# Kernel optimization log

Hardware: AMD Instinct MI355X
Metric: run time of the kernel (lower is better)

## Reference

```python
import jax, jax.numpy as jnp
import numpy as np

B, T, IN, H = 4096, 100, 140, 256


def setup_inputs() -> dict:
    key = jax.random.key(0)
    ks = jax.random.split(key, 13)
    s = 1.0 / np.sqrt(H)  # PyTorch LSTM/Linear default init scale
    u = lambda k, shape: jax.random.uniform(k, shape, jnp.float32, -s, s)
    return {
        "x": jax.random.normal(ks[0], (B, T, IN), jnp.float32),
        # LSTM layer 0 (input 140 -> hidden 256), PyTorch gate order i,f,g,o
        "W_ih0": u(ks[1], (4 * H, IN)),
        "W_hh0": u(ks[2], (4 * H, H)),
        "b_ih0": u(ks[3], (4 * H,)),
        "b_hh0": u(ks[4], (4 * H,)),
        # LSTM layer 1 (hidden 256 -> hidden 256)
        "W_ih1": u(ks[5], (4 * H, H)),
        "W_hh1": u(ks[6], (4 * H, H)),
        "b_ih1": u(ks[7], (4 * H,)),
        "b_hh1": u(ks[8], (4 * H,)),
        # advantage MLP: Linear(256,256) -> ReLU -> Linear(256,1)
        "W_a1": u(ks[9], (H, H)),
        "b_a1": u(ks[10], (H,)),
        "W_a2": u(ks[11], (1, H)),
        "b_a2": u(ks[12], (1,)),
    }


def _lstm_cell(xt, h, c, W_ih, W_hh, b):
    # xt: (B, in), h/c: (B, H). PyTorch gate order: i, f, g, o.
    g = xt @ W_ih.T + h @ W_hh.T + b
    i, f, gg, o = jnp.split(g, 4, axis=-1)
    c_new = jax.nn.sigmoid(f) * c + jax.nn.sigmoid(i) * jnp.tanh(gg)
    h_new = jax.nn.sigmoid(o) * jnp.tanh(c_new)
    return h_new, c_new


def reference(x, W_ih0, W_hh0, b_ih0, b_hh0, W_ih1, W_hh1, b_ih1, b_hh1,
              W_a1, b_a1, W_a2, b_a2):
    Bx = x.shape[0]
    b0 = b_ih0 + b_hh0
    b1 = b_ih1 + b_hh1

    def step(carry, xt):
        h0, c0, h1, c1 = carry
        h0, c0 = _lstm_cell(xt, h0, c0, W_ih0, W_hh0, b0)
        h1, c1 = _lstm_cell(h0, h1, c1, W_ih1, W_hh1, b1)
        a = jax.nn.relu(h1 @ W_a1.T + b_a1) @ W_a2.T + b_a2  # (B, 1)
        return (h0, c0, h1, c1), a[:, 0]

    init = tuple(jnp.zeros((Bx, H), x.dtype) for _ in range(4))
    _, outs = jax.lax.scan(step, init, jnp.swapaxes(x, 0, 1))  # (T, B)
    # Faithful to torch.cat(outputs).view(B, -1): flatten in t-major order,
    # then reshape to (B, T) (this scrambles batch/time exactly as the original).
    return outs.reshape(Bx, -1)
```

## Files before the change

kernel.cpp:

```cpp
#include <hip/hip_runtime.h>
#include <cstdint>
#include <cstddef>

#define T_STEPS 100
#define IN_DIM  140
#define HDIM    256
#define BTOT    4096
#define MROWS   16
#define NBLK    (BTOT/MROWS)
#define NTHR    512

typedef _Float16 f16;
typedef _Float16 f16x8 __attribute__((ext_vector_type(8)));
typedef float    f32x4 __attribute__((ext_vector_type(4)));

#define NS0 13
#define NS1 16
#define NSA 8
#define E0 (NS0*64*512)
#define E1 (NS1*64*512)
#define EA (NSA*16*512)
#define F16TOT (E0+E1+EA)
#define EB 2048
#define PREP_TOT (F16TOT+EB)
#define SL (64*512)

#define ACOLS 680
#define H0COL 160
#define H1COL 416

__device__ __forceinline__ float sigmoidf_(float x) {
    return 1.0f / (1.0f + __expf(-x));
}
__device__ __forceinline__ float tanhf_(float x) {
    return 1.0f - 2.0f / (__expf(2.0f * x) + 1.0f);
}

__global__ void prep(const float* __restrict__ Wih0, const float* __restrict__ Whh0,
                     const float* __restrict__ bih0, const float* __restrict__ bhh0,
                     const float* __restrict__ Wih1, const float* __restrict__ Whh1,
                     const float* __restrict__ bih1, const float* __restrict__ bhh1,
                     const float* __restrict__ Wa1,  f16* __restrict__ wsf,
                     float* __restrict__ wsb)
{
    int idx = blockIdx.x * 256 + threadIdx.x;
    if (idx < E0) {
        int e = idx & 7, l = (idx >> 3) & 63, fi = idx >> 9;
        int nt = fi & 63, ks = fi >> 6;
        int k = ks * 32 + ((l >> 4) << 3) + e;
        int n = nt * 16 + (l & 15);
        float v = (k < 160) ? (k < IN_DIM ? Wih0[n * IN_DIM + k] : 0.f)
                            : Whh0[n * HDIM + (k - 160)];
        wsf[idx] = (f16)v;
    } else if (idx < E0 + E1) {
        int i2 = idx - E0;
        int e = i2 & 7, l = (i2 >> 3) & 63, fi = i2 >> 9;
        int nt = fi & 63, ks = fi >> 6;
        int k = ks * 32 + ((l >> 4) << 3) + e;
        int n = nt * 16 + (l & 15);
        float v = (k < HDIM) ? Wih1[n * HDIM + k] : Whh1[n * HDIM + (k - HDIM)];
        wsf[idx] = (f16)v;
    } else if (idx < F16TOT) {
        int i3 = idx - (E0 + E1);
        int e = i3 & 7, l = (i3 >> 3) & 63, fi = i3 >> 9;
        int nt = fi & 15, ks = fi >> 4;
        int k = ks * 32 + ((l >> 4) << 3) + e;
        int j = nt * 16 + (l & 15);
        wsf[idx] = (f16)Wa1[j * HDIM + k];
    } else if (idx < PREP_TOT) {
        int i4 = idx - F16TOT;
        if (i4 < 1024) wsb[i4] = bih0[i4] + bhh0[i4];
        else           wsb[i4] = bih1[i4 - 1024] + bhh1[i4 - 1024];
    }
}

#define GLOAD_LDS(gsrc, ldst)                                              \
    __builtin_amdgcn_global_load_lds(                                      \
        (const __attribute__((address_space(1))) void*)(gsrc),             \
        (__attribute__((address_space(3))) void*)(ldst), 16, 0, 0)

#define BAR_LG do { asm volatile("s_waitcnt lgkmcnt(0)" ::: "memory");     \
                    __builtin_amdgcn_sched_barrier(0);                     \
                    __builtin_amdgcn_s_barrier();                          \
                    __builtin_amdgcn_sched_barrier(0); } while (0)

__device__ __forceinline__ f16x8 ldfrag(const f16* base, int f, int w, int l) {
    return *(const f16x8*)(base + ((size_t)(((f >> 1) << 4) + 2 * w + (f & 1)) << 9) + l * 8);
}

__global__ __launch_bounds__(NTHR)
__attribute__((amdgpu_waves_per_eu(2)))
void lstm_mfma(
    const float* __restrict__ x, const f16* __restrict__ wsf,
    const float* __restrict__ wsb, const float* __restrict__ Wa2,
    const float* __restrict__ ba1, const float* __restrict__ ba2,
    float* __restrict__ out)
{
    __shared__ __align__(16) f16 A[MROWS][ACOLS];
    __shared__ __align__(16) f16 advL[8 * 16 * 512];
    __shared__ float red[8][MROWS];

    const int tid = threadIdx.x;
    const int l   = tid & 63;
    const int w   = tid >> 6;
    const int lm  = l & 15;
    const int lk  = (l >> 4) << 3;
    const int m0  = (l >> 4) << 2;
    const int row0 = blockIdx.x * MROWS;

    const f16* W0 = wsf;
    const f16* W1 = wsf + E0;
    const f16* WA = wsf + E0 + E1;

    for (int i = tid; i < MROWS * ACOLS; i += NTHR) ((f16*)A)[i] = (f16)0.f;

    const int u0 = (2 * w) * 16 + lm;
    const int u1 = (2 * w + 1) * 16 + lm;
    float b0v[2][4], b1v[2][4];
    #pragma unroll
    for (int g = 0; g < 4; g++) {
        b0v[0][g] = wsb[g * 256 + u0];          b0v[1][g] = wsb[g * 256 + u1];
        b1v[0][g] = wsb[1024 + g * 256 + u0];   b1v[1][g] = wsb[1024 + g * 256 + u1];
    }
    const float bAv[2]  = { ba1[u0], ba1[u1] };
    const float wa2v[2] = { Wa2[u0], Wa2[u1] };
    const float ba2v    = ba2[0];

    #pragma unroll
    for (int fi = 0; fi < 16; fi++) {
        const f16* src = WA + ((size_t)(((fi >> 1) << 4) + 2 * w + (fi & 1)) << 9) + l * 8;
        GLOAD_LDS(src, advL + (size_t)(w * 16 + fi) * 512);
    }

    float c0s[2][4], c1s[2][4];
    #pragma unroll
    for (int q = 0; q < 2; q++)
        #pragma unroll
        for (int r = 0; r < 4; r++) { c0s[q][r] = 0.f; c1s[q][r] = 0.f; }

    for (int i = tid; i < MROWS * IN_DIM; i += NTHR) {
        int b = i / IN_DIM, k = i - b * IN_DIM;
        A[b][k] = (f16)x[(size_t)(row0 + b) * (T_STEPS * IN_DIM) + k];
    }

    f16x8 bsE[8], bsO[8];

#define LDSETX(ARR, BASE)                                                  \
    do { _Pragma("unroll")                                                 \
         for (int f = 0; f < 8; f++) ARR[f] = ldfrag((BASE), f, w, l);     \
    } while (0)

#define MFMA_SX(ARR, COL)                                                  \
    do { f16x8 a0 = *(const f16x8*)&A[lm][(COL) + lk];                     \
         _Pragma("unroll")                                                 \
         for (int g = 0; g < 4; g++)                                       \
             _Pragma("unroll")                                             \
             for (int q = 0; q < 2; q++)                                   \
                 acc[q][g] = __builtin_amdgcn_mfma_f32_16x16x32_f16(       \
                     a0, ARR[g * 2 + q], acc[q][g], 0, 0, 0);              \
    } while (0)

    LDSETX(bsE, W0 + 0 * SL);
    LDSETX(bsO, W0 + 1 * SL);

    __syncthreads();

    #pragma unroll 1
    for (int t = 0; t < T_STEPS; t++) {
        f32x4 acc[2][4];
        #pragma unroll
        for (int q = 0; q < 2; q++)
            #pragma unroll
            for (int g = 0; g < 4; g++) {
                float b = b0v[q][g];
                acc[q][g] = (f32x4){b, b, b, b};
            }
        #pragma unroll 1
        for (int j = 0; j < 5; j++) {
            MFMA_SX(bsE, (2 * j) * 32);     LDSETX(bsE, W0 + (size_t)(2 * j + 2) * SL);
            MFMA_SX(bsO, (2 * j + 1) * 32); LDSETX(bsO, W0 + (size_t)(2 * j + 3) * SL);
        }
        MFMA_SX(bsE, 10 * 32);  LDSETX(bsE, W0 + 12 * SL);
        MFMA_SX(bsO, 11 * 32);  LDSETX(bsO, W1 + 1 * SL);
        MFMA_SX(bsE, 12 * 32);  LDSETX(bsE, W1 + 0 * SL);

        f16 hnew[2][4];
        #pragma unroll
        for (int q = 0; q < 2; q++)
            #pragma unroll
            for (int r = 0; r < 4; r++) {
                float ig = sigmoidf_(acc[q][0][r]);
                float fg = sigmoidf_(acc[q][1][r]);
                float gv = tanhf_   (acc[q][2][r]);
                float og = sigmoidf_(acc[q][3][r]);
                float c  = fmaf(fg, c0s[q][r], ig * gv);
                c0s[q][r] = c;
                hnew[q][r] = (f16)(og * tanhf_(c));
            }
        BAR_LG;
        #pragma unroll
        for (int r = 0; r < 4; r++) {
            A[m0 + r][H0COL + u0] = hnew[0][r];
            A[m0 + r][H0COL + u1] = hnew[1][r];
        }
        BAR_LG;

        #pragma unroll
        for (int q = 0; q < 2; q++)
            #pragma unroll
            for (int g = 0; g < 4; g++) {
                float b = b1v[q][g];
                acc[q][g] = (f32x4){b, b, b, b};
            }
        #pragma unroll 1
        for (int j = 0; j < 7; j++) {
            MFMA_SX(bsE, H0COL + (2 * j) * 32);     LDSETX(bsE, W1 + (size_t)(2 * j + 2) * SL);
            MFMA_SX(bsO, H0COL + (2 * j + 1) * 32); LDSETX(bsO, W1 + (size_t)(2 * j + 3) * SL);
        }
        MFMA_SX(bsE, H0COL + 14 * 32);  LDSETX(bsE, W0 + 0 * SL);
        MFMA_SX(bsO, H0COL + 15 * 32);  LDSETX(bsO, W0 + 1 * SL);

        #pragma unroll
        for (int q = 0; q < 2; q++)
            #pragma unroll
            for (int r = 0; r < 4; r++) {
                float ig = sigmoidf_(acc[q][0][r]);
                float fg = sigmoidf_(acc[q][1][r]);
                float gv = tanhf_   (acc[q][2][r]);
                float og = sigmoidf_(acc[q][3][r]);
                float c  = fmaf(fg, c1s[q][r], ig * gv);
                c1s[q][r] = c;
                hnew[q][r] = (f16)(og * tanhf_(c));
            }
        BAR_LG;
        #pragma unroll
        for (int r = 0; r < 4; r++) {
            A[m0 + r][H1COL + u0] = hnew[0][r];
            A[m0 + r][H1COL + u1] = hnew[1][r];
        }
        BAR_LG;

        f32x4 accA[2];
        #pragma unroll
        for (int q = 0; q < 2; q++) {
            float b = bAv[q];
            accA[q] = (f32x4){b, b, b, b};
        }
        #pragma unroll
        for (int ks = 0; ks < NSA; ks++) {
            f16x8 a0 = *(const f16x8*)&A[lm][H1COL + ks * 32 + lk];
            f16x8 bf0 = *(const f16x8*)(advL + (size_t)(w * 16 + 2 * ks + 0) * 512 + l * 8);
            f16x8 bf1 = *(const f16x8*)(advL + (size_t)(w * 16 + 2 * ks + 1) * 512 + l * 8);
            accA[0] = __builtin_amdgcn_mfma_f32_16x16x32_f16(a0, bf0, accA[0], 0, 0, 0);
            accA[1] = __builtin_amdgcn_mfma_f32_16x16x32_f16(a0, bf1, accA[1], 0, 0, 0);
        }

        {
            const int tn = (t + 1 < T_STEPS) ? (t + 1) : t;
            for (int i = tid; i < MROWS * IN_DIM; i += NTHR) {
                int b = i / IN_DIM, k = i - b * IN_DIM;
                A[b][k] = (f16)x[(size_t)(row0 + b) * (T_STEPS * IN_DIM) + (size_t)tn * IN_DIM + k];
            }
        }

        float s[4];
        #pragma unroll
        for (int r = 0; r < 4; r++)
            s[r] = fmaxf(accA[0][r], 0.f) * wa2v[0] + fmaxf(accA[1][r], 0.f) * wa2v[1];
        #pragma unroll
        for (int msk = 1; msk < 16; msk <<= 1)
            #pragma unroll
            for (int r = 0; r < 4; r++)
                s[r] += __shfl_xor(s[r], msk, 64);
        if (lm == 0) {
            #pragma unroll
            for (int r = 0; r < 4; r++) red[w][m0 + r] = s[r];
        }
        BAR_LG;
        if (tid < MROWS) {
            float o = ba2v;
            #pragma unroll
            for (int w2 = 0; w2 < 8; w2++) o += red[w2][tid];
            out[(size_t)t * BTOT + row0 + tid] = o;
        }
    }
#undef LDSETX
#undef MFMA_SX
}

extern "C" void kernel_launch(void* const* d_in, const int* in_sizes, int n_in,
                              void* d_out, int out_size, void* d_ws, size_t ws_size,
                              hipStream_t stream)
{
    const float* x    = (const float*)d_in[0];
    const float* Wih0 = (const float*)d_in[1];
    const float* Whh0 = (const float*)d_in[2];
    const float* bih0 = (const float*)d_in[3];
    const float* bhh0 = (const float*)d_in[4];
    const float* Wih1 = (const float*)d_in[5];
    const float* Whh1 = (const float*)d_in[6];
    const float* bih1 = (const float*)d_in[7];
    const float* bhh1 = (const float*)d_in[8];
    const float* Wa1  = (const float*)d_in[9];
    const float* ba1  = (const float*)d_in[10];
    const float* Wa2  = (const float*)d_in[11];
    const float* ba2  = (const float*)d_in[12];

    f16*   wsf = (f16*)d_ws;
    float* wsb = (float*)((char*)d_ws + (size_t)F16TOT * sizeof(f16));
    float* out = (float*)d_out;

    hipLaunchKernelGGL(prep, dim3(PREP_TOT / 256), dim3(256), 0, stream,
                       Wih0, Whh0, bih0, bhh0, Wih1, Whh1, bih1, bhh1, Wa1, wsf, wsb);
    hipLaunchKernelGGL(lstm_mfma, dim3(NBLK), dim3(NTHR), 0, stream,
                       x, wsf, wsb, Wa2, ba1, ba2, out);
}
```

Measured before the change: 1.854 ms.

## Split hidden units across 16 waves instead of 8 per block

Doubles the block to 1024 threads so each wave owns one 16-unit hidden slice instead of two. Per-wave MFMA work, weight fragments and register state are halved, and the advantage-MLP reduction now sums over 16 waves. The aim is more latency hiding and parallelism within the serial recurrence. In exchange each wave streams its own weight fragments, so the A-operand LDS reads are duplicated, barriers span twice as many waves, and the waves_per_eu hint is removed, which may change occupancy.

Measured after the change: 1.943 ms. +4.8%, slower.

```diff
diff --git a/kernel.cpp b/kernel.cpp
--- a/kernel.cpp
+++ b/kernel.cpp
@@ -8,7 +8,7 @@
 #define BTOT    4096
 #define MROWS   16
 #define NBLK    (BTOT/MROWS)
-#define NTHR    512
+#define NTHR    1024
 
 typedef _Float16 f16;
 typedef _Float16 f16x8 __attribute__((ext_vector_type(8)));
@@ -84,12 +84,7 @@
                     __builtin_amdgcn_s_barrier();                          \
                     __builtin_amdgcn_sched_barrier(0); } while (0)
 
-__device__ __forceinline__ f16x8 ldfrag(const f16* base, int f, int w, int l) {
-    return *(const f16x8*)(base + ((size_t)(((f >> 1) << 4) + 2 * w + (f & 1)) << 9) + l * 8);
-}
-
 __global__ __launch_bounds__(NTHR)
-__attribute__((amdgpu_waves_per_eu(2)))
 void lstm_mfma(
     const float* __restrict__ x, const f16* __restrict__ wsf,
     const float* __restrict__ wsb, const float* __restrict__ Wa2,
@@ -97,8 +92,8 @@
     float* __restrict__ out)
 {
     __shared__ __align__(16) f16 A[MROWS][ACOLS];
-    __shared__ __align__(16) f16 advL[8 * 16 * 512];
-    __shared__ float red[8][MROWS];
+    __shared__ __align__(16) f16 advL[16 * 8 * 512];
+    __shared__ float red[16][MROWS];
 
     const int tid = threadIdx.x;
     const int l   = tid & 63;
@@ -114,50 +109,47 @@
 
     for (int i = tid; i < MROWS * ACOLS; i += NTHR) ((f16*)A)[i] = (f16)0.f;
 
-    const int u0 = (2 * w) * 16 + lm;
-    const int u1 = (2 * w + 1) * 16 + lm;
-    float b0v[2][4], b1v[2][4];
+    const int u = w * 16 + lm;
+    float b0v[4], b1v[4];
     #pragma unroll
     for (int g = 0; g < 4; g++) {
-        b0v[0][g] = wsb[g * 256 + u0];          b0v[1][g] = wsb[g * 256 + u1];
-        b1v[0][g] = wsb[1024 + g * 256 + u0];   b1v[1][g] = wsb[1024 + g * 256 + u1];
-    }
-    const float bAv[2]  = { ba1[u0], ba1[u1] };
-    const float wa2v[2] = { Wa2[u0], Wa2[u1] };
-    const float ba2v    = ba2[0];
+        b0v[g] = wsb[g * 256 + u];
+        b1v[g] = wsb[1024 + g * 256 + u];
+    }
+    const float bAv  = ba1[u];
+    const float wa2v = Wa2[u];
+    const float ba2v = ba2[0];
 
     #pragma unroll
-    for (int fi = 0; fi < 16; fi++) {
-        const f16* src = WA + ((size_t)(((fi >> 1) << 4) + 2 * w + (fi & 1)) << 9) + l * 8;
-        GLOAD_LDS(src, advL + (size_t)(w * 16 + fi) * 512);
-    }
-
-    float c0s[2][4], c1s[2][4];
+    for (int ks = 0; ks < NSA; ks++) {
+        const f16* src = WA + ((size_t)(ks * 16 + w)) * 512 + l * 8;
+        GLOAD_LDS(src, advL + (size_t)(w * 8 + ks) * 512);
+    }
+
+    float c0s[4], c1s[4];
     #pragma unroll
-    for (int q = 0; q < 2; q++)
-        #pragma unroll
-        for (int r = 0; r < 4; r++) { c0s[q][r] = 0.f; c1s[q][r] = 0.f; }
+    for (int r = 0; r < 4; r++) { c0s[r] = 0.f; c1s[r] = 0.f; }
 
     for (int i = tid; i < MROWS * IN_DIM; i += NTHR) {
         int b = i / IN_DIM, k = i - b * IN_DIM;
         A[b][k] = (f16)x[(size_t)(row0 + b) * (T_STEPS * IN_DIM) + k];
     }
 
-    f16x8 bsE[8], bsO[8];
+    f16x8 bsE[4], bsO[4];
 
 #define LDSETX(ARR, BASE)                                                  \
     do { _Pragma("unroll")                                                 \
-         for (int f = 0; f < 8; f++) ARR[f] = ldfrag((BASE), f, w, l);     \
+         for (int g = 0; g < 4; g++)                                       \
+             ARR[g] = *(const f16x8*)((BASE) +                             \
+                        ((size_t)((g << 4) + w) << 9) + l * 8);            \
     } while (0)
 
 #define MFMA_SX(ARR, COL)                                                  \
     do { f16x8 a0 = *(const f16x8*)&A[lm][(COL) + lk];                     \
          _Pragma("unroll")                                                 \
          for (int g = 0; g < 4; g++)                                       \
-             _Pragma("unroll")                                             \
-             for (int q = 0; q < 2; q++)                                   \
-                 acc[q][g] = __builtin_amdgcn_mfma_f32_16x16x32_f16(       \
-                     a0, ARR[g * 2 + q], acc[q][g], 0, 0, 0);              \
+             acc[g] = __builtin_amdgcn_mfma_f32_16x16x32_f16(              \
+                 a0, ARR[g], acc[g], 0, 0, 0);                             \
     } while (0)
 
     LDSETX(bsE, W0 + 0 * SL);
@@ -167,14 +159,12 @@
 
     #pragma unroll 1
     for (int t = 0; t < T_STEPS; t++) {
-        f32x4 acc[2][4];
-        #pragma unroll
-        for (int q = 0; q < 2; q++)
-            #pragma unroll
-            for (int g = 0; g < 4; g++) {
-                float b = b0v[q][g];
-                acc[q][g] = (f32x4){b, b, b, b};
-            }
+        f32x4 acc[4];
+        #pragma unroll
+        for (int g = 0; g < 4; g++) {
+            float b = b0v[g];
+            acc[g] = (f32x4){b, b, b, b};
+        }
         #pragma unroll 1
         for (int j = 0; j < 5; j++) {
             MFMA_SX(bsE, (2 * j) * 32);     LDSETX(bsE, W0 + (size_t)(2 * j + 2) * SL);
@@ -184,34 +174,28 @@
         MFMA_SX(bsO, 11 * 32);  LDSETX(bsO, W1 + 1 * SL);
         MFMA_SX(bsE, 12 * 32);  LDSETX(bsE, W1 + 0 * SL);
 
-        f16 hnew[2][4];
-        #pragma unroll
-        for (int q = 0; q < 2; q++)
-            #pragma unroll
-            for (int r = 0; r < 4; r++) {
-                float ig = sigmoidf_(acc[q][0][r]);
-                float fg = sigmoidf_(acc[q][1][r]);
-                float gv = tanhf_   (acc[q][2][r]);
-                float og = sigmoidf_(acc[q][3][r]);
-                float c  = fmaf(fg, c0s[q][r], ig * gv);
-                c0s[q][r] = c;
-                hnew[q][r] = (f16)(og * tanhf_(c));
-            }
-        BAR_LG;
+        f16 hnew[4];
         #pragma unroll
         for (int r = 0; r < 4; r++) {
-            A[m0 + r][H0COL + u0] = hnew[0][r];
-            A[m0 + r][H0COL + u1] = hnew[1][r];
-        }
-        BAR_LG;
-
-        #pragma unroll
-        for (int q = 0; q < 2; q++)
-            #pragma unroll
-            for (int g = 0; g < 4; g++) {
-                float b = b1v[q][g];
-                acc[q][g] = (f32x4){b, b, b, b};
-            }
+            float ig = sigmoidf_(acc[0][r]);
+            float fg = sigmoidf_(acc[1][r]);
+            float gv = tanhf_   (acc[2][r]);
+            float og = sigmoidf_(acc[3][r]);
+            float c  = fmaf(fg, c0s[r], ig * gv);
+            c0s[r] = c;
+            hnew[r] = (f16)(og * tanhf_(c));
+        }
+        BAR_LG;
+        #pragma unroll
+        for (int r = 0; r < 4; r++)
+            A[m0 + r][H0COL + u] = hnew[r];
+        BAR_LG;
+
+        #pragma unroll
+        for (int g = 0; g < 4; g++) {
+            float b = b1v[g];
+            acc[g] = (f32x4){b, b, b, b};
+        }
         #pragma unroll 1
         for (int j = 0; j < 7; j++) {
             MFMA_SX(bsE, H0COL + (2 * j) * 32);     LDSETX(bsE, W1 + (size_t)(2 * j + 2) * SL);
@@ -221,38 +205,27 @@
         MFMA_SX(bsO, H0COL + 15 * 32);  LDSETX(bsO, W0 + 1 * SL);
 
         #pragma unroll
-        for (int q = 0; q < 2; q++)
-            #pragma unroll
-            for (int r = 0; r < 4; r++) {
-                float ig = sigmoidf_(acc[q][0][r]);
-                float fg = sigmoidf_(acc[q][1][r]);
-                float gv = tanhf_   (acc[q][2][r]);
-                float og = sigmoidf_(acc[q][3][r]);
-                float c  = fmaf(fg, c1s[q][r], ig * gv);
-                c1s[q][r] = c;
-                hnew[q][r] = (f16)(og * tanhf_(c));
-            }
-        BAR_LG;
-        #pragma unroll
         for (int r = 0; r < 4; r++) {
-            A[m0 + r][H1COL + u0] = hnew[0][r];
-            A[m0 + r][H1COL + u1] = hnew[1][r];
-        }
-        BAR_LG;
-
-        f32x4 accA[2];
-        #pragma unroll
-        for (int q = 0; q < 2; q++) {
-            float b = bAv[q];
-            accA[q] = (f32x4){b, b, b, b};
-        }
+            float ig = sigmoidf_(acc[0][r]);
+            float fg = sigmoidf_(acc[1][r]);
+            float gv = tanhf_   (acc[2][r]);
+            float og = sigmoidf_(acc[3][r]);
+            float c  = fmaf(fg, c1s[r], ig * gv);
+            c1s[r] = c;
+            hnew[r] = (f16)(og * tanhf_(c));
+        }
+        BAR_LG;
+        #pragma unroll
+        for (int r = 0; r < 4; r++)
+            A[m0 + r][H1COL + u] = hnew[r];
+        BAR_LG;
+
+        f32x4 accA = (f32x4){bAv, bAv, bAv, bAv};
         #pragma unroll
         for (int ks = 0; ks < NSA; ks++) {
             f16x8 a0 = *(const f16x8*)&A[lm][H1COL + ks * 32 + lk];
-            f16x8 bf0 = *(const f16x8*)(advL + (size_t)(w * 16 + 2 * ks + 0) * 512 + l * 8);
-            f16x8 bf1 = *(const f16x8*)(advL + (size_t)(w * 16 + 2 * ks + 1) * 512 + l * 8);
-            accA[0] = __builtin_amdgcn_mfma_f32_16x16x32_f16(a0, bf0, accA[0], 0, 0, 0);
-            accA[1] = __builtin_amdgcn_mfma_f32_16x16x32_f16(a0, bf1, accA[1], 0, 0, 0);
+            f16x8 bf = *(const f16x8*)(advL + (size_t)(w * 8 + ks) * 512 + l * 8);
+            accA = __builtin_amdgcn_mfma_f32_16x16x32_f16(a0, bf, accA, 0, 0, 0);
         }
 
         {
@@ -266,7 +239,7 @@
         float s[4];
         #pragma unroll
         for (int r = 0; r < 4; r++)
-            s[r] = fmaxf(accA[0][r], 0.f) * wa2v[0] + fmaxf(accA[1][r], 0.f) * wa2v[1];
+            s[r] = fmaxf(accA[r], 0.f) * wa2v;
         #pragma unroll
         for (int msk = 1; msk < 16; msk <<= 1)
             #pragma unroll
@@ -280,7 +253,7 @@
         if (tid < MROWS) {
             float o = ba2v;
             #pragma unroll
-            for (int w2 = 0; w2 < 8; w2++) o += red[w2][tid];
+            for (int w2 = 0; w2 < 16; w2++) o += red[w2][tid];
             out[(size_t)t * BTOT + row0 + tid] = o;
         }
     }
```
